# Kernel optimization log

Hardware: AMD Instinct MI355X
Metric: run time of the kernel (lower is better)

Reference implementation:

```python
import jax, jax.numpy as jnp
import numpy as np

L, N, D = 2, 100000, 128
TRACE_HID, MVC_DIM, MVC_HID = 256, 128, 64
NUM_EDGE = 1600000
TAU = 0.5


def setup_inputs() -> dict:
    key = jax.random.key(0)
    ks = jax.random.split(key, 9)
    trace_all = jax.random.normal(ks[0], (L, N, D), dtype=jnp.float32)
    W_lin = jax.random.normal(ks[1], (TRACE_HID, L * D), dtype=jnp.float32) * 0.05
    W_lin2 = jax.random.normal(ks[2], (MVC_DIM, TRACE_HID), dtype=jnp.float32) * 0.05
    W_fc1 = jax.random.normal(ks[3], (MVC_HID, 2 * MVC_DIM), dtype=jnp.float32) * 0.05
    b_fc1 = jax.random.normal(ks[4], (MVC_HID,), dtype=jnp.float32) * 0.05
    W_fc2 = jax.random.normal(ks[5], (2, MVC_HID), dtype=jnp.float32) * 0.05
    b_fc2 = jax.random.normal(ks[6], (2,), dtype=jnp.float32) * 0.05
    u = jax.random.uniform(ks[7], (NUM_EDGE, 2), dtype=jnp.float32, minval=1e-6, maxval=1.0 - 1e-6)
    gumbel = -jnp.log(-jnp.log(u))  # standard Gumbel(0,1) noise
    edge_index = jax.random.randint(ks[8], (2, 3 * NUM_EDGE), 0, N, dtype=jnp.int32)
    return {
        "trace_all": trace_all, "W_lin": W_lin, "W_lin2": W_lin2,
        "W_fc1": W_fc1, "b_fc1": b_fc1, "W_fc2": W_fc2, "b_fc2": b_fc2,
        "gumbel": gumbel, "edge_index": edge_index, "num_edge": NUM_EDGE,
    }


def reference(trace_all, W_lin, W_lin2, W_fc1, b_fc1, W_fc2, b_fc2, gumbel, edge_index, num_edge):
    # --- TraceMLP: [L, N, d] -> mvc [N, mvc_dim] (eval mode: dropout is identity)
    l, n, d = trace_all.shape
    x = jnp.transpose(trace_all, (1, 0, 2)).reshape(n, l * d)      # [N, L*d]
    h = jax.nn.relu(x @ W_lin.T)                                   # [N, trace_hidden]
    mvc = h @ W_lin2.T                                             # [N, mvc_dim]
    norm = jnp.maximum(jnp.linalg.norm(mvc, axis=1, keepdims=True), 1e-12)
    mvc = mvc / norm                                               # F.normalize(p=2, dim=1)

    # --- EdgeScoringNet over non-slow edges (first num_edge columns)
    src = edge_index[0, :num_edge]
    dst = edge_index[1, :num_edge]
    comb = jnp.concatenate([mvc[src], mvc[dst]], axis=1)           # [E, 2*mvc_dim]
    h2 = jax.nn.relu(comb @ W_fc1.T + b_fc1)                       # [E, mvc_hidden]
    scores = h2 @ W_fc2.T + b_fc2                                  # [E, 2]

    # --- gumbel_softmax(tau=0.5, hard=True)[:, 0] (straight-through)
    y_soft = jax.nn.softmax((scores + gumbel) / TAU, axis=-1)
    y_hard = jax.nn.one_hot(jnp.argmax(y_soft, axis=-1), 2, dtype=y_soft.dtype)
    ret = y_hard - jax.lax.stop_gradient(y_soft) + y_soft
    active = ret[:, 0]                                             # [E], values in {0,1}

    # --- train_mask: first block = active, next two blocks = 1 - active
    train_mask = jnp.concatenate([active, 1.0 - active, 1.0 - active])  # [3*E]
    return train_mask
```

## Files before the change

kernel.cpp:

```cpp
#include <hip/hip_runtime.h>

#define NN   100000
#define EE   1600000
#define EROW 4800000

typedef _Float16 half8 __attribute__((ext_vector_type(8)));
typedef _Float16 half4 __attribute__((ext_vector_type(4)));
typedef float    f32x4 __attribute__((ext_vector_type(4)));

__device__ __forceinline__ float4 ld4(const float* p){ return *(const float4*)p; }

__device__ __forceinline__ unsigned splitf(float v) {
    _Float16 h = (_Float16)v;
    float r = v - (float)h;
    _Float16 l = (_Float16)(r * 2048.0f);
    union { _Float16 f; unsigned short u; } uh, ul;
    uh.f = h; ul.f = l;
    return (unsigned)uh.u | ((unsigned)ul.u << 16);
}

__global__ __launch_bounds__(256)
void prep_w(const float* __restrict__ W1, const float* __restrict__ W2,
            const float* __restrict__ W3, unsigned* __restrict__ o1,
            unsigned* __restrict__ o2, unsigned* __restrict__ o3)
{
    int idx = blockIdx.x * 256 + threadIdx.x;
    if (idx < 65536) {
        o1[idx] = splitf(W1[idx]);
    } else if (idx < 98304) {
        int i = idx - 65536;
        o2[i] = splitf(W2[i]);
    } else {
        int i = idx - 98304;
        int j = i >> 7, k = i & 127;
        o3[i] = splitf(W3[(j & 63) * 256 + (j >> 6) * 128 + k]);
    }
}

template<int SRCA, int EPI, int K>
__global__ __launch_bounds__(256, 2)
void gemm_mfma(const void* __restrict__ Asrc, const unsigned* __restrict__ Bw,
               const float* __restrict__ bias, unsigned* __restrict__ outS,
               float* __restrict__ outF, unsigned short* __restrict__ outH,
               int M, int No)
{
    __shared__ float sqv[128][2];

    const int t     = threadIdx.x;
    const int wm    = (t >> 6) >> 1;
    const int wn    = (t >> 6) & 1;
    const int lane  = t & 63;
    const int lm    = lane & 15;
    const int q     = lane >> 4;
    const int mBase = blockIdx.x * 128;
    const int nBase = blockIdx.y * 128;

    f32x4 aH[4][4], aM[4][4];
#pragma unroll
    for (int i = 0; i < 4; ++i)
#pragma unroll
        for (int j = 0; j < 4; ++j) {
            aH[i][j] = (f32x4){0.f, 0.f, 0.f, 0.f};
            aM[i][j] = (f32x4){0.f, 0.f, 0.f, 0.f};
        }

    int arow[4], brow[4];
#pragma unroll
    for (int i = 0; i < 4; ++i) {
        int r = mBase + wm * 64 + i * 16 + lm;
        arow[i] = r < M ? r : M - 1;
        brow[i] = nBase + wn * 64 + i * 16 + lm;
    }

    union HL { uint4 u; half8 h; };

#pragma unroll
    for (int kt = 0; kt < K / 32; ++kt) {
        const int k0 = kt * 32 + q * 8;

        half8 fAh[4], fAl[4], fBh[4], fBl[4];

#pragma unroll
        for (int i = 0; i < 4; ++i) {
            HL H, L;
            if (SRCA == 0) {
                const float* ap = (const float*)Asrc
                    + (size_t)(k0 >> 7) * ((size_t)NN * 128)
                    + (size_t)arow[i] * 128 + (k0 & 127);
                float4 f0 = ld4(ap);
                float4 f1 = ld4(ap + 4);
                unsigned p0 = splitf(f0.x), p1 = splitf(f0.y);
                unsigned p2 = splitf(f0.z), p3 = splitf(f0.w);
                unsigned p4 = splitf(f1.x), p5 = splitf(f1.y);
                unsigned p6 = splitf(f1.z), p7 = splitf(f1.w);
                H.u.x = (p0 & 0xffffu) | (p1 << 16);
                H.u.y = (p2 & 0xffffu) | (p3 << 16);
                H.u.z = (p4 & 0xffffu) | (p5 << 16);
                H.u.w = (p6 & 0xffffu) | (p7 << 16);
                L.u.x = (p0 >> 16) | (p1 & 0xffff0000u);
                L.u.y = (p2 >> 16) | (p3 & 0xffff0000u);
                L.u.z = (p4 >> 16) | (p5 & 0xffff0000u);
                L.u.w = (p6 >> 16) | (p7 & 0xffff0000u);
            } else {
                const unsigned* ap = (const unsigned*)Asrc + (size_t)arow[i] * K + k0;
                uint4 u0 = *(const uint4*)ap;
                uint4 u1 = *(const uint4*)(ap + 4);
                H.u.x = (u0.x & 0xffffu) | (u0.y << 16);
                H.u.y = (u0.z & 0xffffu) | (u0.w << 16);
                H.u.z = (u1.x & 0xffffu) | (u1.y << 16);
                H.u.w = (u1.z & 0xffffu) | (u1.w << 16);
                L.u.x = (u0.x >> 16) | (u0.y & 0xffff0000u);
                L.u.y = (u0.z >> 16) | (u0.w & 0xffff0000u);
                L.u.z = (u1.x >> 16) | (u1.y & 0xffff0000u);
                L.u.w = (u1.z >> 16) | (u1.w & 0xffff0000u);
            }
            fAh[i] = H.h;
            fAl[i] = L.h;
        }

#pragma unroll
        for (int j = 0; j < 4; ++j) {
            const unsigned* bp = Bw + (size_t)brow[j] * K + k0;
            uint4 u0 = *(const uint4*)bp;
            uint4 u1 = *(const uint4*)(bp + 4);
            HL H, L;
            H.u.x = (u0.x & 0xffffu) | (u0.y << 16);
            H.u.y = (u0.z & 0xffffu) | (u0.w << 16);
            H.u.z = (u1.x & 0xffffu) | (u1.y << 16);
            H.u.w = (u1.z & 0xffffu) | (u1.w << 16);
            L.u.x = (u0.x >> 16) | (u0.y & 0xffff0000u);
            L.u.y = (u0.z >> 16) | (u0.w & 0xffff0000u);
            L.u.z = (u1.x >> 16) | (u1.y & 0xffff0000u);
            L.u.w = (u1.z >> 16) | (u1.w & 0xffff0000u);
            fBh[j] = H.h;
            fBl[j] = L.h;
        }

        __builtin_amdgcn_s_setprio(1);
#pragma unroll
        for (int i = 0; i < 4; ++i)
#pragma unroll
            for (int j = 0; j < 4; ++j)
                aH[i][j] = __builtin_amdgcn_mfma_f32_16x16x32_f16(fAh[i], fBh[j], aH[i][j], 0, 0, 0);
#pragma unroll
        for (int i = 0; i < 4; ++i)
#pragma unroll
            for (int j = 0; j < 4; ++j)
                aM[i][j] = __builtin_amdgcn_mfma_f32_16x16x32_f16(fAh[i], fBl[j], aM[i][j], 0, 0, 0);
#pragma unroll
        for (int i = 0; i < 4; ++i)
#pragma unroll
            for (int j = 0; j < 4; ++j)
                aM[i][j] = __builtin_amdgcn_mfma_f32_16x16x32_f16(fAl[i], fBh[j], aM[i][j], 0, 0, 0);
        __builtin_amdgcn_s_setprio(0);
    }

    const float cM = 1.0f / 2048.0f;
#pragma unroll
    for (int i = 0; i < 4; ++i)
#pragma unroll
        for (int j = 0; j < 4; ++j)
            aH[i][j] = aH[i][j] + aM[i][j] * cM;

    float nm[4][4];
    if (EPI == 1) {
#pragma unroll
        for (int i = 0; i < 4; ++i)
#pragma unroll
            for (int r = 0; r < 4; ++r) {
                float s = 0.f;
#pragma unroll
                for (int j = 0; j < 4; ++j) { float x = aH[i][j][r]; s = fmaf(x, x, s); }
#pragma unroll
                for (int off = 1; off < 16; off <<= 1) s += __shfl_xor(s, off, 16);
                if (lm == 0) sqv[wm * 64 + i * 16 + q * 4 + r][wn] = s;
            }
        __syncthreads();
#pragma unroll
        for (int i = 0; i < 4; ++i)
#pragma unroll
            for (int r = 0; r < 4; ++r) {
                const int rl = wm * 64 + i * 16 + q * 4 + r;
                nm[i][r] = fmaxf(sqrtf(sqv[rl][0] + sqv[rl][1]), 1e-12f);
            }
    }

    float bj[4] = {0.f, 0.f, 0.f, 0.f};
    if (EPI == 2 && wn == 0) {
#pragma unroll
        for (int j = 0; j < 4; ++j) bj[j] = bias[j * 16 + lm];
    }

#pragma unroll
    for (int i = 0; i < 4; ++i)
#pragma unroll
        for (int r = 0; r < 4; ++r) {
            const int m = mBase + wm * 64 + i * 16 + q * 4 + r;
            if (m < M) {
#pragma unroll
                for (int j = 0; j < 4; ++j) {
                    const int c = nBase + wn * 64 + j * 16 + lm;
                    float v = aH[i][j][r];
                    if (EPI == 0) { v = fmaxf(v, 0.f); outS[(size_t)m * No + c] = splitf(v); }
                    if (EPI == 1) { v = v / nm[i][r];  outS[(size_t)m * No + c] = splitf(v); }
                    if (EPI == 2) {
                        v += bj[j];
                        outF[(size_t)m * No + c] = v;
                        union { _Float16 f; unsigned short u; } cv; cv.f = (_Float16)v;
                        outH[(size_t)m * No + c] = cv.u;
                    }
                }
            }
        }
}

#define EPB 128
__global__ __launch_bounds__(256, 4)
void edge_k(const unsigned short* __restrict__ pH, const float* __restrict__ p,
            const int* __restrict__ ei, const float* __restrict__ gum,
            const float* __restrict__ W2, const float* __restrict__ b2,
            float* __restrict__ out)
{
    __shared__ int   sidx[EPB];
    __shared__ int   didx[EPB];
    __shared__ float gl[2 * EPB];
    __shared__ float act[EPB];

    const int t  = threadIdx.x;
    const int e0 = blockIdx.x * EPB;

    if (t < EPB) sidx[t] = ei[e0 + t];
    else         didx[t - EPB] = ei[EROW + e0 + (t - EPB)];
    gl[t] = gum[(size_t)e0 * 2 + t];
    __syncthreads();

    const int j   = t & 15;
    const int grp = t >> 4;
    const float4 w0 = ld4(&W2[j * 4]);
    const float4 w1 = ld4(&W2[64 + j * 4]);
    const float4 dk = make_float4(w0.x - w1.x, w0.y - w1.y,
                                  w0.z - w1.z, w0.w - w1.w);
    const float4 dw = make_float4(fabsf(dk.x), fabsf(dk.y),
                                  fabsf(dk.z), fabsf(dk.w));
    const float b20 = b2[0], b21 = b2[1];
    const float dB  = b20 - b21;

    union U8 { uint2 u; half4 h; };
    U8 ua[8], ub[8];
#pragma unroll
    for (int it = 0; it < 8; ++it) {
        const int el = grp * 8 + it;
        ua[it].u = *(const uint2*)&pH[(size_t)sidx[el] * 128 + j * 4];
        ub[it].u = *(const uint2*)&pH[(size_t)didx[el] * 128 + 64 + j * 4];
    }

#pragma unroll
    for (int it = 0; it < 8; ++it) {
        const int el = grp * 8 + it;
        const float a0 = (float)ua[it].h[0], a1 = (float)ua[it].h[1];
        const float a2 = (float)ua[it].h[2], a3 = (float)ua[it].h[3];
        const float c0 = (float)ub[it].h[0], c1 = (float)ub[it].h[1];
        const float c2 = (float)ub[it].h[2], c3 = (float)ub[it].h[3];
        const float r0 = fmaxf(a0 + c0, 0.f);
        const float r1 = fmaxf(a1 + c1, 0.f);
        const float r2 = fmaxf(a2 + c2, 0.f);
        const float r3 = fmaxf(a3 + c3, 0.f);
        float sc = r0 * dk.x + r1 * dk.y + r2 * dk.z + r3 * dk.w;
        float eb = dw.x * (fabsf(a0) + fabsf(c0)) + dw.y * (fabsf(a1) + fabsf(c1))
                 + dw.z * (fabsf(a2) + fabsf(c2)) + dw.w * (fabsf(a3) + fabsf(c3));
#pragma unroll
        for (int off = 1; off < 16; off <<= 1) {
            sc += __shfl_xor(sc, off, 16);
            eb += __shfl_xor(eb, off, 16);
        }
        const float g0 = gl[el * 2], g1 = gl[el * 2 + 1];
        const float gap = sc + dB + (g0 - g1);
        const float bound = eb * 0.0009765625f + 2e-5f;
        float av;
        if (fabsf(gap) > bound) {
            av = (gap >= 0.f) ? 1.f : 0.f;
        } else {
            const float4 pa = ld4(&p[(size_t)sidx[el] * 128 + j * 4]);
            const float4 pb = ld4(&p[(size_t)didx[el] * 128 + 64 + j * 4]);
            const float q0 = fmaxf(pa.x + pb.x, 0.f);
            const float q1 = fmaxf(pa.y + pb.y, 0.f);
            const float q2 = fmaxf(pa.z + pb.z, 0.f);
            const float q3 = fmaxf(pa.w + pb.w, 0.f);
            float t0 = q0 * w0.x + q1 * w0.y + q2 * w0.z + q3 * w0.w;
            float t1 = q0 * w1.x + q1 * w1.y + q2 * w1.z + q3 * w1.w;
#pragma unroll
            for (int off = 1; off < 16; off <<= 1) {
                t0 += __shfl_xor(t0, off, 16);
                t1 += __shfl_xor(t1, off, 16);
            }
            const float ge = (t0 + b20 + g0) - (t1 + b21 + g1);
            av = (ge >= 0.f) ? 1.f : 0.f;
        }
        if (j == 0) act[el] = av;
    }
    __syncthreads();

    if (t < EPB) {
        const float a = act[t];
        const size_t e = (size_t)e0 + t;
        out[e]                  = a;
        out[EE + e]             = 1.f - a;
        out[2 * (size_t)EE + e] = 1.f - a;
    }
}

extern "C" void kernel_launch(void* const* d_in, const int* in_sizes, int n_in,
                              void* d_out, int out_size, void* d_ws, size_t ws_size,
                              hipStream_t stream)
{
    const float* trace  = (const float*)d_in[0];
    const float* W_lin  = (const float*)d_in[1];
    const float* W_lin2 = (const float*)d_in[2];
    const float* W_fc1  = (const float*)d_in[3];
    const float* b_fc1  = (const float*)d_in[4];
    const float* W_fc2  = (const float*)d_in[5];
    const float* b_fc2  = (const float*)d_in[6];
    const float* gum    = (const float*)d_in[7];
    const int*   ei     = (const int*)  d_in[8];
    float*       out    = (float*)d_out;

    char* ws = (char*)d_ws;
    unsigned*       hpl = (unsigned*)ws;
    unsigned*       mpl = (unsigned*)(ws + (size_t)NN * 256 * 4);
    unsigned*       W1i = (unsigned*)(ws + (size_t)NN * 256 * 4 + (size_t)NN * 128 * 4);
    unsigned*       W2i = W1i + 65536;
    unsigned*       W3i = W2i + 32768;
    float*          p   = (float*)ws;
    unsigned short* pH  = (unsigned short*)(ws + (size_t)NN * 128 * 4);

    prep_w<<<448, 256, 0, stream>>>(W_lin, W_lin2, W_fc1, W1i, W2i, W3i);

    const int mB = (NN + 127) / 128;

    gemm_mfma<0, 0, 256><<<dim3(mB, 2), 256, 0, stream>>>(trace, W1i, nullptr, hpl, nullptr, nullptr, NN, 256);
    gemm_mfma<1, 1, 256><<<dim3(mB, 1), 256, 0, stream>>>(hpl, W2i, nullptr, mpl, nullptr, nullptr, NN, 128);
    gemm_mfma<1, 2, 128><<<dim3(mB, 1), 256, 0, stream>>>(mpl, W3i, b_fc1, nullptr, p, pH, NN, 128);
    edge_k<<<EE / EPB, 256, 0, stream>>>(pH, p, ei, gum, W_fc2, b_fc2, out);
}
```

Baseline: 434.7 us.

## Stage GEMM tiles through double-buffered LDS with async global_load_lds

Operand tiles of A and B are no longer loaded by each wave straight from global memory. They are now copied into shared memory with the direct global-to-LDS load instruction, using a double buffer over the K loop and an XOR-swizzled layout to avoid bank conflicts. Each tile is fetched once per block instead of once per wave that needs it, and the next tile's fetch overlaps the current MFMA work. In exchange it adds 64KB of LDS per block, which may lower occupancy under the two-blocks-per-CU launch bound, and a barrier on every K step.

```diff
diff --git a/kernel.cpp b/kernel.cpp
--- a/kernel.cpp
+++ b/kernel.cpp
@@ -17,6 +17,13 @@
     union { _Float16 f; unsigned short u; } uh, ul;
     uh.f = h; ul.f = l;
     return (unsigned)uh.u | ((unsigned)ul.u << 16);
+}
+
+__device__ __forceinline__ void dma16(const void* g, void* l) {
+    __builtin_amdgcn_global_load_lds(
+        (const __attribute__((address_space(1))) unsigned*)((size_t)g),
+        (__attribute__((address_space(3))) unsigned*)((size_t)l),
+        16, 0, 0);
 }
 
 __global__ __launch_bounds__(256)
@@ -44,17 +51,22 @@
                float* __restrict__ outF, unsigned short* __restrict__ outH,
                int M, int No)
 {
+    __shared__ __align__(16) unsigned bufA[2][128 * 32];
+    __shared__ __align__(16) unsigned bufB[2][128 * 32];
     __shared__ float sqv[128][2];
 
     const int t     = threadIdx.x;
-    const int wm    = (t >> 6) >> 1;
-    const int wn    = (t >> 6) & 1;
+    const int w     = t >> 6;
+    const int wm    = w >> 1;
+    const int wn    = w & 1;
     const int lane  = t & 63;
     const int lm    = lane & 15;
     const int q     = lane >> 4;
     const int mBase = blockIdx.x * 128;
     const int nBase = blockIdx.y * 128;
 
+    const int col16 = (lane & 7) ^ (lane >> 3);
+
     f32x4 aH[4][4], aM[4][4];
 #pragma unroll
     for (int i = 0; i < 4; ++i)
@@ -64,31 +76,54 @@
             aM[i][j] = (f32x4){0.f, 0.f, 0.f, 0.f};
         }
 
-    int arow[4], brow[4];
-#pragma unroll
-    for (int i = 0; i < 4; ++i) {
-        int r = mBase + wm * 64 + i * 16 + lm;
-        arow[i] = r < M ? r : M - 1;
-        brow[i] = nBase + wn * 64 + i * 16 + lm;
-    }
+    auto stage = [&](int sb, int kt) {
+#pragma unroll
+        for (int c = 0; c < 4; ++c) {
+            const int row = w * 32 + c * 8 + (lane >> 3);
+            unsigned* ldsA = &bufA[sb][w * 1024 + c * 256];
+            unsigned* ldsB = &bufB[sb][w * 1024 + c * 256];
+            int rgA = mBase + row; rgA = rgA < M ? rgA : M - 1;
+            if (SRCA == 0) {
+                const int kg    = kt * 32;
+                const int plane = kg >> 7;
+                const int ktl   = kg & 127;
+                const float* gA = (const float*)Asrc
+                    + (size_t)plane * ((size_t)NN * 128)
+                    + (size_t)rgA * 128 + ktl + col16 * 4;
+                dma16(gA, ldsA);
+            } else {
+                const unsigned* gA = (const unsigned*)Asrc
+                    + (size_t)rgA * K + kt * 32 + col16 * 4;
+                dma16(gA, ldsA);
+            }
+            const unsigned* gB = Bw + (size_t)(nBase + row) * K + kt * 32 + col16 * 4;
+            dma16(gB, ldsB);
+        }
+    };
 
     union HL { uint4 u; half8 h; };
 
-#pragma unroll
-    for (int kt = 0; kt < K / 32; ++kt) {
-        const int k0 = kt * 32 + q * 8;
+    constexpr int NK = K / 32;
+    stage(0, 0);
+    __syncthreads();
+
+#pragma unroll 2
+    for (int kt = 0; kt < NK; ++kt) {
+        const int b = kt & 1;
+        if (kt + 1 < NK) stage(b ^ 1, kt + 1);
 
         half8 fAh[4], fAl[4], fBh[4], fBl[4];
 
 #pragma unroll
         for (int i = 0; i < 4; ++i) {
+            const int r = wm * 64 + i * 16 + lm;
+            const int x = r & 7;
+            const unsigned* p0p = &bufA[b][r * 32 + (((2 * q) ^ x) << 2)];
+            const unsigned* p1p = &bufA[b][r * 32 + ((((2 * q) | 1) ^ x) << 2)];
             HL H, L;
             if (SRCA == 0) {
-                const float* ap = (const float*)Asrc
-                    + (size_t)(k0 >> 7) * ((size_t)NN * 128)
-                    + (size_t)arow[i] * 128 + (k0 & 127);
-                float4 f0 = ld4(ap);
-                float4 f1 = ld4(ap + 4);
+                float4 f0 = *(const float4*)p0p;
+                float4 f1 = *(const float4*)p1p;
                 unsigned p0 = splitf(f0.x), p1 = splitf(f0.y);
                 unsigned p2 = splitf(f0.z), p3 = splitf(f0.w);
                 unsigned p4 = splitf(f1.x), p5 = splitf(f1.y);
@@ -102,9 +137,8 @@
                 L.u.z = (p4 >> 16) | (p5 & 0xffff0000u);
                 L.u.w = (p6 >> 16) | (p7 & 0xffff0000u);
             } else {
-                const unsigned* ap = (const unsigned*)Asrc + (size_t)arow[i] * K + k0;
-                uint4 u0 = *(const uint4*)ap;
-                uint4 u1 = *(const uint4*)(ap + 4);
+                uint4 u0 = *(const uint4*)p0p;
+                uint4 u1 = *(const uint4*)p1p;
                 H.u.x = (u0.x & 0xffffu) | (u0.y << 16);
                 H.u.y = (u0.z & 0xffffu) | (u0.w << 16);
                 H.u.z = (u1.x & 0xffffu) | (u1.y << 16);
@@ -120,9 +154,10 @@
 
 #pragma unroll
         for (int j = 0; j < 4; ++j) {
-            const unsigned* bp = Bw + (size_t)brow[j] * K + k0;
-            uint4 u0 = *(const uint4*)bp;
-            uint4 u1 = *(const uint4*)(bp + 4);
+            const int r = wn * 64 + j * 16 + lm;
+            const int x = r & 7;
+            uint4 u0 = *(const uint4*)&bufB[b][r * 32 + (((2 * q) ^ x) << 2)];
+            uint4 u1 = *(const uint4*)&bufB[b][r * 32 + ((((2 * q) | 1) ^ x) << 2)];
             HL H, L;
             H.u.x = (u0.x & 0xffffu) | (u0.y << 16);
             H.u.y = (u0.z & 0xffffu) | (u0.w << 16);
@@ -153,6 +188,8 @@
             for (int j = 0; j < 4; ++j)
                 aM[i][j] = __builtin_amdgcn_mfma_f32_16x16x32_f16(fAl[i], fBh[j], aM[i][j], 0, 0, 0);
         __builtin_amdgcn_s_setprio(0);
+
+        if (kt + 1 < NK) __syncthreads();
     }
 
     const float cM = 1.0f / 2048.0f;
```

New measurement: 369.9 us. -14.9%, faster.
